# Optimization experiments

Hardware: AMD Instinct MI355X
Metric: run time of the kernel (lower is better)

Reference implementation:

```python
import jax, jax.numpy as jnp
import numpy as np

N = 50000          # nodes
E = 800000         # edges per metapath
P = 4              # metapaths
IN = 256           # in_size
D = 32 * 8         # out_size * layer_num_heads = 256
SEM_H = 128        # SemanticAttention hidden


def setup_inputs() -> dict:
    key = jax.random.key(0)
    ks = jax.random.split(key, 8)
    h = jax.random.normal(ks[0], (N, IN), dtype=jnp.float32)
    src = jax.random.randint(ks[1], (P, E), 0, N, dtype=jnp.int32)
    dst = jax.random.randint(ks[2], (P, E), 0, N, dtype=jnp.int32)
    # per-metapath GraphConv weights (Glorot-ish scale)
    W_gc = jax.random.normal(ks[3], (P, IN, D), dtype=jnp.float32) / np.sqrt(IN)
    b_gc = jnp.zeros((P, D), dtype=jnp.float32)
    # SemanticAttention: Linear(D, SEM_H) -> tanh -> Linear(SEM_H, 1, bias=False)
    W1 = jax.random.normal(ks[4], (D, SEM_H), dtype=jnp.float32) / np.sqrt(D)
    b1 = jnp.zeros((SEM_H,), dtype=jnp.float32)
    w2 = jax.random.normal(ks[5], (SEM_H,), dtype=jnp.float32) / np.sqrt(SEM_H)
    return {"h": h, "src": src, "dst": dst, "W_gc": W_gc, "b_gc": b_gc,
            "W1": W1, "b1": b1, "w2": w2}


def _graph_conv(h, src, dst, W, b):
    # DGL GraphConv with norm='both': D_dst^{-1/2} A D_src^{-1/2} (h W) + b
    ones = jnp.ones((src.shape[0],), dtype=h.dtype)
    deg_out = jnp.clip(jax.ops.segment_sum(ones, src, num_segments=N), 1.0)
    deg_in = jnp.clip(jax.ops.segment_sum(ones, dst, num_segments=N), 1.0)
    x = (h @ W) * jax.lax.rsqrt(deg_out)[:, None]          # [N, D]
    agg = jax.ops.segment_sum(x[src], dst, num_segments=N)  # gather-scatter [N, D]
    return agg * jax.lax.rsqrt(deg_in)[:, None] + b


def reference(h, src, dst, W_gc, b_gc, W1, b1, w2):
    # per-metapath GraphConv (fixed small loop over P metapaths)
    zs = [_graph_conv(h, src[p], dst[p], W_gc[p], b_gc[p]) for p in range(P)]
    z = jnp.stack(zs, axis=1)                               # [N, P, D]
    # SemanticAttention: project -> mean over nodes -> softmax over metapaths
    s = jnp.tanh(z @ W1 + b1) @ w2                          # [N, P]
    beta = jax.nn.softmax(s.mean(axis=0), axis=0)           # [P]
    return jnp.einsum('npd,p->nd', z, beta)                 # [N, D]
```

## Files before the change

kernel.cpp:

```cpp
#include <hip/hip_runtime.h>

#define NN 50000
#define NE 800000
#define NP 4
#define DIN 256
#define DD 256
#define NH 128
#define SA 40
#define NSEG 16
#define SEGE (NE / NSEG)
#define FCH 8192
#define NFC 7
#define SPAD(k) ((k) + ((k) >> 5))

typedef __attribute__((ext_vector_type(8))) short bf16x8;
typedef __attribute__((ext_vector_type(4))) float f32x4;

__device__ __forceinline__ unsigned short f2bf(float f) {
  unsigned u = __float_as_uint(f);
  u += 0x7fff + ((u >> 16) & 1);
  return (unsigned short)(u >> 16);
}
__device__ __forceinline__ float bfl(unsigned u) { return __uint_as_float(u << 16); }
__device__ __forceinline__ float bfh(unsigned u) { return __uint_as_float(u & 0xffff0000u); }


__global__ __launch_bounds__(256) void hist2d_kernel(const int* __restrict__ idx,
                                                     int* __restrict__ cnt) {
  int bx = blockIdx.x;
  int c = bx % NFC, s = bx / NFC;
  int p = blockIdx.y;
  int base = c * FCH, nk = min(FCH, NN - base);
  __shared__ int hs[FCH];
  for (int k = threadIdx.x; k < FCH; k += 256) hs[k] = 0;
  __syncthreads();
  const int4* a4 = (const int4*)(idx + (size_t)p * NE + (size_t)s * SEGE);
  for (int i = threadIdx.x; i < SEGE / 4; i += 256) {
    int4 v = a4[i];
    int k;
    k = v.x - base; if ((unsigned)k < (unsigned)nk) atomicAdd(&hs[k], 1);
    k = v.y - base; if ((unsigned)k < (unsigned)nk) atomicAdd(&hs[k], 1);
    k = v.z - base; if ((unsigned)k < (unsigned)nk) atomicAdd(&hs[k], 1);
    k = v.w - base; if ((unsigned)k < (unsigned)nk) atomicAdd(&hs[k], 1);
  }
  __syncthreads();
  int* out = cnt + (size_t)(p * NSEG + s) * NN + base;
  for (int k = threadIdx.x; k < nk; k += 256) out[k] = hs[k];
}


__global__ __launch_bounds__(1024) void scanA_kernel(
    int* __restrict__ cntD, const int* __restrict__ cntS,
    float* __restrict__ rin, float* __restrict__ rout,
    int* __restrict__ row_ptr, int* __restrict__ chunkdeg) {
  int c = blockIdx.x, p = blockIdx.y;
  int base = c * FCH, nk = min(FCH, NN - base);
  __shared__ int sdeg[FCH + (FCH >> 5)];
  __shared__ int wtot[16], wexc[16];
  int t = threadIdx.x;
  for (int kk = t; kk < FCH; kk += 1024) {
    int run = 0;
    if (kk < nk) {
      size_t o = (size_t)(p * NSEG) * NN + base + kk;
      for (int s = 0; s < NSEG; ++s) {
        size_t oo = o + (size_t)s * NN;
        int v = cntD[oo];
        cntD[oo] = run;
        run += v;
      }
      rin[(size_t)p * NN + base + kk] = rsqrtf((float)max(run, 1));
      int rs = 0;
      for (int s = 0; s < NSEG; ++s) rs += cntS[o + (size_t)s * NN];
      rout[(size_t)p * NN + base + kk] = rsqrtf((float)max(rs, 1));
    }
    sdeg[SPAD(kk)] = run;
  }
  __syncthreads();
  int loc[8];
  int ssum = 0;
#pragma unroll
  for (int j = 0; j < 8; ++j) { loc[j] = ssum; ssum += sdeg[SPAD(t * 8 + j)]; }
  int incl = ssum;
  int lane = t & 63, w = t >> 6;
#pragma unroll
  for (int o = 1; o < 64; o <<= 1) {
    int v = __shfl_up(incl, o);
    if (lane >= o) incl += v;
  }
  if (lane == 63) wtot[w] = incl;
  __syncthreads();
  if (t == 0) {
    int r = 0;
    for (int i = 0; i < 16; ++i) { wexc[i] = r; r += wtot[i]; }
  }
  __syncthreads();
  int tbase = wexc[w] + incl - ssum;
  int* rp = row_ptr + (size_t)p * (NN + 1) + base;
#pragma unroll
  for (int j = 0; j < 8; ++j) {
    int k = t * 8 + j;
    if (k < nk) rp[k] = tbase + loc[j];
  }
  if (t == 1023) chunkdeg[p * NFC + c] = tbase + ssum;
}


__global__ void scanB_kernel(const int* __restrict__ chunkdeg, int* __restrict__ chunk_base,
                             int* __restrict__ row_ptr) {
  int t = threadIdx.x;
  if (t < NP) {
    int run = 0;
    for (int c = 0; c < NFC; ++c) { chunk_base[t * NFC + c] = run; run += chunkdeg[t * NFC + c]; }
    row_ptr[(size_t)t * (NN + 1) + NN] = NE;
  }
}

__global__ __launch_bounds__(1024) void rpfin_kernel(int* __restrict__ row_ptr,
                                                     const int* __restrict__ chunk_base) {
  int k = blockIdx.x * 1024 + threadIdx.x, p = blockIdx.y;
  if (k < NN) row_ptr[(size_t)p * (NN + 1) + k] += chunk_base[p * NFC + (k >> 13)];
}


__global__ __launch_bounds__(256) void scatter_kernel(
    const int* __restrict__ src, const int* __restrict__ dst,
    const int* __restrict__ cntD, const int* __restrict__ row_ptr, int* __restrict__ col) {
  int bx = blockIdx.x;
  int c = bx % NFC, s = bx / NFC;
  int p = blockIdx.y;
  int base = c * FCH, nk = min(FCH, NN - base);
  __shared__ int cur[FCH];
  for (int k = threadIdx.x; k < nk; k += 256)
    cur[k] = row_ptr[(size_t)p * (NN + 1) + base + k] +
             cntD[(size_t)(p * NSEG + s) * NN + base + k];
  __syncthreads();
  const int4* d4 = (const int4*)(dst + (size_t)p * NE + (size_t)s * SEGE);
  const int4* s4 = (const int4*)(src + (size_t)p * NE + (size_t)s * SEGE);
  int* colp = col + (size_t)p * NE;
  for (int i = threadIdx.x; i < SEGE / 4; i += 256) {
    int4 dv = d4[i];
    int4 sv = s4[i];
    int k;
    k = dv.x - base; if ((unsigned)k < (unsigned)nk) colp[atomicAdd(&cur[k], 1)] = sv.x;
    k = dv.y - base; if ((unsigned)k < (unsigned)nk) colp[atomicAdd(&cur[k], 1)] = sv.y;
    k = dv.z - base; if ((unsigned)k < (unsigned)nk) colp[atomicAdd(&cur[k], 1)] = sv.z;
    k = dv.w - base; if ((unsigned)k < (unsigned)nk) colp[atomicAdd(&cur[k], 1)] = sv.w;
  }
}


__global__ void cvt_h_kernel(const float4* __restrict__ h4, ushort4* __restrict__ h2) {
  int i = blockIdx.x * blockDim.x + threadIdx.x;
  if (i >= NN * DIN / 4) return;
  float4 v = h4[i];
  ushort4 o;
  o.x = f2bf(v.x); o.y = f2bf(v.y); o.z = f2bf(v.z); o.w = f2bf(v.w);
  h2[i] = o;
}


__global__ __launch_bounds__(256) void agg_kernel(
    const ushort* __restrict__ h2, const int* __restrict__ col,
    const int* __restrict__ row_ptr, const float* __restrict__ rout,
    const float* __restrict__ rin, ushort* __restrict__ g) {
  int p = blockIdx.y;
  int v = blockIdx.x * 4 + (threadIdx.x >> 6);
  int lane = threadIdx.x & 63;
  const int* colp = col + (size_t)p * NE;
  const float* rop = rout + (size_t)p * NN;
  int beg = row_ptr[p * (NN + 1) + v], end = row_ptr[p * (NN + 1) + v + 1];
  const uint2* hv = (const uint2*)h2;
  float a0 = 0, a1 = 0, a2 = 0, a3 = 0, b0 = 0, b1 = 0, b2 = 0, b3 = 0;
  int j = beg;
  for (; j + 1 < end; j += 2) {
    int s0 = colp[j], s1 = colp[j + 1];
    float r0 = rop[s0], r1 = rop[s1];
    uint2 u0 = hv[(size_t)s0 * 64 + lane];
    uint2 u1 = hv[(size_t)s1 * 64 + lane];
    a0 = fmaf(r0, bfl(u0.x), a0); a1 = fmaf(r0, bfh(u0.x), a1);
    a2 = fmaf(r0, bfl(u0.y), a2); a3 = fmaf(r0, bfh(u0.y), a3);
    b0 = fmaf(r1, bfl(u1.x), b0); b1 = fmaf(r1, bfh(u1.x), b1);
    b2 = fmaf(r1, bfl(u1.y), b2); b3 = fmaf(r1, bfh(u1.y), b3);
  }
  if (j < end) {
    int s0 = colp[j];
    float r0 = rop[s0];
    uint2 u0 = hv[(size_t)s0 * 64 + lane];
    a0 = fmaf(r0, bfl(u0.x), a0); a1 = fmaf(r0, bfh(u0.x), a1);
    a2 = fmaf(r0, bfl(u0.y), a2); a3 = fmaf(r0, bfh(u0.y), a3);
  }
  float ri = rin[(size_t)p * NN + v];
  ushort4 o;
  o.x = f2bf((a0 + b0) * ri); o.y = f2bf((a1 + b1) * ri);
  o.z = f2bf((a2 + b2) * ri); o.w = f2bf((a3 + b3) * ri);
  ((ushort4*)(g + ((size_t)p * NN + v) * DIN))[lane] = o;
}


__global__ void wmul_kernel(const float* __restrict__ Wgc, const float* __restrict__ W1,
                            ushort* __restrict__ Mt) {
  int p = blockIdx.y, k = blockIdx.x, j = threadIdx.x;
  const float* wrow = Wgc + ((size_t)p * DIN + k) * DD;
  float s = 0.f;
  for (int d = 0; d < DD; ++d) s = fmaf(wrow[d], W1[(size_t)d * NH + j], s);
  Mt[((size_t)p * NH + j) * DIN + k] = f2bf(s);
}

__global__ void cvec_kernel(const float* __restrict__ bgc, const float* __restrict__ W1,
                            const float* __restrict__ b1, float* __restrict__ cvec) {
  int p = blockIdx.x, j = threadIdx.x;
  const float* b = bgc + (size_t)p * DD;
  float s = b1[j];
  for (int d = 0; d < DD; ++d) s = fmaf(b[d], W1[(size_t)d * NH + j], s);
  cvec[p * NH + j] = s;
}


__global__ __launch_bounds__(256) void gemm_sem(
    const ushort* __restrict__ g, const ushort* __restrict__ Mt,
    const float* __restrict__ cvec, const float* __restrict__ w2,
    float* __restrict__ ssum) {
  __shared__ ushort As[128 * SA];
  __shared__ ushort Bs[128 * SA];
  __shared__ float wsumf[4];
  const int tid = threadIdx.x;
  const int p = blockIdx.y;
  const int row0 = blockIdx.x * 128;
  const int wave = tid >> 6, lane = tid & 63;
  const int wr = wave >> 1, wc = wave & 1;
  const int srow = tid >> 2, sseg = tid & 3;
  const int fr = lane & 15, fk = (lane >> 4) * 8;
  const ushort* Ag = g + (size_t)p * NN * DIN;
  const ushort* Bg = Mt + (size_t)p * NH * DIN;
  int ar0 = row0 + srow; if (ar0 >= NN) ar0 = NN - 1;
  int ar1 = row0 + srow + 64; if (ar1 >= NN) ar1 = NN - 1;
  f32x4 acc[4][4] = {};
  for (int k2 = 0; k2 < DIN; k2 += 32) {
    uint4 av0 = *(const uint4*)(Ag + (size_t)ar0 * DIN + k2 + sseg * 8);
    uint4 av1 = *(const uint4*)(Ag + (size_t)ar1 * DIN + k2 + sseg * 8);
    uint4 bv0 = *(const uint4*)(Bg + (size_t)srow * DIN + k2 + sseg * 8);
    uint4 bv1 = *(const uint4*)(Bg + (size_t)(srow + 64) * DIN + k2 + sseg * 8);
    __syncthreads();
    *(uint4*)&As[srow * SA + sseg * 8] = av0;
    *(uint4*)&As[(srow + 64) * SA + sseg * 8] = av1;
    *(uint4*)&Bs[srow * SA + sseg * 8] = bv0;
    *(uint4*)&Bs[(srow + 64) * SA + sseg * 8] = bv1;
    __syncthreads();
    bf16x8 af[4], bfv[4];
#pragma unroll
    for (int t = 0; t < 4; ++t) {
      af[t] = *(const bf16x8*)&As[(wr * 64 + t * 16 + fr) * SA + fk];
      bfv[t] = *(const bf16x8*)&Bs[(wc * 64 + t * 16 + fr) * SA + fk];
    }
#pragma unroll
    for (int mt = 0; mt < 4; ++mt)
#pragma unroll
      for (int nt = 0; nt < 4; ++nt)
        acc[mt][nt] = __builtin_amdgcn_mfma_f32_16x16x32_bf16(af[mt], bfv[nt], acc[mt][nt], 0, 0, 0);
  }
  float s = 0.f;
#pragma unroll
  for (int nt = 0; nt < 4; ++nt) {
    int c = wc * 64 + nt * 16 + fr;
    float cc = cvec[p * NH + c];
    float ww = w2[c];
#pragma unroll
    for (int mt = 0; mt < 4; ++mt)
#pragma unroll
      for (int i = 0; i < 4; ++i) {
        int r = row0 + wr * 64 + mt * 16 + (lane >> 4) * 4 + i;
        if (r < NN) {
          float x = acc[mt][nt][i] + cc;
          x = fminf(fmaxf(x, -15.f), 15.f);
          float e = __expf(2.f * x);
          s = fmaf((e - 1.f) / (e + 1.f), ww, s);
        }
      }
  }
#pragma unroll
  for (int o = 32; o > 0; o >>= 1) s += __shfl_down(s, o);
  if (lane == 0) wsumf[wave] = s;
  __syncthreads();
  if (tid == 0) atomicAdd(&ssum[p], wsumf[0] + wsumf[1] + wsumf[2] + wsumf[3]);
}


__global__ void beta_kernel(const float* __restrict__ ssum, const float* __restrict__ bgc,
                            float* __restrict__ beta, float* __restrict__ bout) {
  __shared__ float sb[NP];
  if (threadIdx.x == 0) {
    float m[NP];
    float mx = -1e30f;
    for (int p = 0; p < NP; ++p) {
      m[p] = ssum[p] / (float)NN;
      mx = fmaxf(mx, m[p]);
    }
    float tot = 0.f;
    for (int p = 0; p < NP; ++p) { m[p] = expf(m[p] - mx); tot += m[p]; }
    for (int p = 0; p < NP; ++p) { sb[p] = m[p] / tot; beta[p] = sb[p]; }
  }
  __syncthreads();
  int d = threadIdx.x;
  float s = 0.f;
  for (int p = 0; p < NP; ++p) s = fmaf(sb[p], bgc[p * DD + d], s);
  bout[d] = s;
}

__global__ void scaleWt_kernel(const float* __restrict__ Wgc, const float* __restrict__ beta,
                               ushort* __restrict__ Wt) {
  int i = blockIdx.x * blockDim.x + threadIdx.x;
  if (i >= DD * NP * DIN) return;
  int n = i >> 10;
  int pk = i & 1023;
  int p = pk >> 8, k = pk & 255;
  Wt[i] = f2bf(beta[p] * Wgc[((size_t)p * DIN + k) * DD + n]);
}


__global__ __launch_bounds__(256) void gemm_main(
    const ushort* __restrict__ g, const ushort* __restrict__ Wt,
    const float* __restrict__ bout, float* __restrict__ out) {
  __shared__ ushort As[128 * SA];
  __shared__ ushort Bs[128 * SA];
  const int tid = threadIdx.x;
  const int row0 = blockIdx.x * 128;
  const int col0 = blockIdx.y * 128;
  const int wave = tid >> 6, lane = tid & 63;
  const int wr = wave >> 1, wc = wave & 1;
  const int srow = tid >> 2, sseg = tid & 3;
  const int fr = lane & 15, fk = (lane >> 4) * 8;
  int ar0 = row0 + srow; if (ar0 >= NN) ar0 = NN - 1;
  int ar1 = row0 + srow + 64; if (ar1 >= NN) ar1 = NN - 1;
  f32x4 acc[4][4] = {};
  for (int p = 0; p < NP; ++p) {
    const ushort* Ag = g + (size_t)p * NN * DIN;
    for (int k2 = 0; k2 < DIN; k2 += 32) {
      uint4 av0 = *(const uint4*)(Ag + (size_t)ar0 * DIN + k2 + sseg * 8);
      uint4 av1 = *(const uint4*)(Ag + (size_t)ar1 * DIN + k2 + sseg * 8);
      uint4 bv0 = *(const uint4*)(Wt + (size_t)(col0 + srow) * (NP * DIN) + p * DIN + k2 + sseg * 8);
      uint4 bv1 = *(const uint4*)(Wt + (size_t)(col0 + srow + 64) * (NP * DIN) + p * DIN + k2 + sseg * 8);
      __syncthreads();
      *(uint4*)&As[srow * SA + sseg * 8] = av0;
      *(uint4*)&As[(srow + 64) * SA + sseg * 8] = av1;
      *(uint4*)&Bs[srow * SA + sseg * 8] = bv0;
      *(uint4*)&Bs[(srow + 64) * SA + sseg * 8] = bv1;
      __syncthreads();
      bf16x8 af[4], bfv[4];
#pragma unroll
      for (int t = 0; t < 4; ++t) {
        af[t] = *(const bf16x8*)&As[(wr * 64 + t * 16 + fr) * SA + fk];
        bfv[t] = *(const bf16x8*)&Bs[(wc * 64 + t * 16 + fr) * SA + fk];
      }
#pragma unroll
      for (int mt = 0; mt < 4; ++mt)
#pragma unroll
        for (int nt = 0; nt < 4; ++nt)
          acc[mt][nt] = __builtin_amdgcn_mfma_f32_16x16x32_bf16(af[mt], bfv[nt], acc[mt][nt], 0, 0, 0);
    }
  }
#pragma unroll
  for (int nt = 0; nt < 4; ++nt) {
    int c = col0 + wc * 64 + nt * 16 + fr;
    float bb = bout[c];
#pragma unroll
    for (int mt = 0; mt < 4; ++mt)
#pragma unroll
      for (int i = 0; i < 4; ++i) {
        int r = row0 + wr * 64 + mt * 16 + (lane >> 4) * 4 + i;
        if (r < NN) out[(size_t)r * DD + c] = acc[mt][nt][i] + bb;
      }
  }
}


extern "C" void kernel_launch(void* const* d_in, const int* in_sizes, int n_in,
                              void* d_out, int out_size, void* d_ws, size_t ws_size,
                              hipStream_t stream) {
  const float* h = (const float*)d_in[0];
  const int* src = (const int*)d_in[1];
  const int* dst = (const int*)d_in[2];
  const float* Wgc = (const float*)d_in[3];
  const float* bgc = (const float*)d_in[4];
  const float* W1 = (const float*)d_in[5];
  const float* b1 = (const float*)d_in[6];
  const float* w2 = (const float*)d_in[7];
  float* out = (float*)d_out;

  char* base = (char*)d_ws;
  size_t off = 0;
  auto alloc = [&](size_t bytes) -> char* {
    char* ptr = base + off;
    off = (off + bytes + 255) & ~(size_t)255;
    return ptr;
  };
  int* cntD = (int*)alloc((size_t)NP * NSEG * NN * sizeof(int));
  int* cntS = (int*)alloc((size_t)NP * NSEG * NN * sizeof(int));
  float* rin = (float*)alloc((size_t)NP * NN * sizeof(float));
  float* rout = (float*)alloc((size_t)NP * NN * sizeof(float));
  int* row_ptr = (int*)alloc((size_t)NP * (NN + 1) * sizeof(int));
  int* chunkdeg = (int*)alloc((size_t)NP * NFC * sizeof(int));
  int* chunk_base = (int*)alloc((size_t)NP * NFC * sizeof(int));
  ushort* h2 = (ushort*)alloc((size_t)NN * DIN * sizeof(ushort));
  ushort* g = (ushort*)alloc((size_t)NP * NN * DIN * sizeof(ushort));
  ushort* Mt = (ushort*)alloc((size_t)NP * NH * DIN * sizeof(ushort));
  ushort* Wt = (ushort*)alloc((size_t)DD * NP * DIN * sizeof(ushort));
  float* cvec = (float*)alloc((size_t)NP * NH * sizeof(float));
  float* ssum = (float*)alloc(NP * sizeof(float));
  float* beta = (float*)alloc(NP * sizeof(float));
  float* bout = (float*)alloc(DD * sizeof(float));
  int* colbuf = (int*)cntS;
  if (off > ws_size) return;

  hipMemsetAsync(ssum, 0, NP * sizeof(float), stream);

  hist2d_kernel<<<dim3(NFC * NSEG, NP), 256, 0, stream>>>(dst, cntD);
  hist2d_kernel<<<dim3(NFC * NSEG, NP), 256, 0, stream>>>(src, cntS);
  scanA_kernel<<<dim3(NFC, NP), 1024, 0, stream>>>(cntD, cntS, rin, rout, row_ptr, chunkdeg);
  scanB_kernel<<<1, 64, 0, stream>>>(chunkdeg, chunk_base, row_ptr);
  rpfin_kernel<<<dim3((NN + 1023) / 1024, NP), 1024, 0, stream>>>(row_ptr, chunk_base);
  cvt_h_kernel<<<(NN * DIN / 4 + 255) / 256, 256, 0, stream>>>((const float4*)h, (ushort4*)h2);
  scatter_kernel<<<dim3(NFC * NSEG, NP), 256, 0, stream>>>(src, dst, cntD, row_ptr, colbuf);
  agg_kernel<<<dim3(NN / 4, NP), 256, 0, stream>>>(h2, colbuf, row_ptr, rout, rin, g);
  wmul_kernel<<<dim3(DIN, NP), NH, 0, stream>>>(Wgc, W1, Mt);
  cvec_kernel<<<NP, NH, 0, stream>>>(bgc, W1, b1, cvec);
  gemm_sem<<<dim3((NN + 127) / 128, NP), 256, 0, stream>>>(g, Mt, cvec, w2, ssum);
  beta_kernel<<<1, 256, 0, stream>>>(ssum, bgc, beta, bout);
  scaleWt_kernel<<<(DD * NP * DIN + 255) / 256, 256, 0, stream>>>(Wgc, beta, Wt);
  gemm_main<<<dim3((NN + 127) / 128, 2), 256, 0, stream>>>(g, Wt, bout, out);
}
```

Before: 656.6 us.

## Use global-atomic CSR build, batched-index gather with packed FMA, reorder GEMM grid

Replaces the segmented shared-memory histogram and scatter, which scan all edges seven times per chunk, with single-pass global-atomic degree counting and a global-atomic scatter into a separate column buffer. The aggregation kernel now stages up to 64 neighbor indices and weights per wave in shared memory, issues 8 gathers at once, and accumulates with packed v_pk_fma_f32. The main GEMM grid is transposed so the two column tiles of a row block run next to each other and can share A in L2. The cost is global atomic contention and a nondeterministic edge order within each CSR row, plus two extra memsets.

```diff
diff --git a/kernel.cpp b/kernel.cpp
--- a/kernel.cpp
+++ b/kernel.cpp
@@ -7,50 +7,51 @@
 #define DD 256
 #define NH 128
 #define SA 40
-#define NSEG 16
-#define SEGE (NE / NSEG)
 #define FCH 8192
 #define NFC 7
 #define SPAD(k) ((k) + ((k) >> 5))
 
 typedef __attribute__((ext_vector_type(8))) short bf16x8;
 typedef __attribute__((ext_vector_type(4))) float f32x4;
+typedef __attribute__((ext_vector_type(2))) float f32x2;
 
 __device__ __forceinline__ unsigned short f2bf(float f) {
   unsigned u = __float_as_uint(f);
   u += 0x7fff + ((u >> 16) & 1);
   return (unsigned short)(u >> 16);
 }
-__device__ __forceinline__ float bfl(unsigned u) { return __uint_as_float(u << 16); }
-__device__ __forceinline__ float bfh(unsigned u) { return __uint_as_float(u & 0xffff0000u); }
-
-
-__global__ __launch_bounds__(256) void hist2d_kernel(const int* __restrict__ idx,
-                                                     int* __restrict__ cnt) {
-  int bx = blockIdx.x;
-  int c = bx % NFC, s = bx / NFC;
-  int p = blockIdx.y;
-  int base = c * FCH, nk = min(FCH, NN - base);
-  __shared__ int hs[FCH];
-  for (int k = threadIdx.x; k < FCH; k += 256) hs[k] = 0;
-  __syncthreads();
-  const int4* a4 = (const int4*)(idx + (size_t)p * NE + (size_t)s * SEGE);
-  for (int i = threadIdx.x; i < SEGE / 4; i += 256) {
-    int4 v = a4[i];
-    int k;
-    k = v.x - base; if ((unsigned)k < (unsigned)nk) atomicAdd(&hs[k], 1);
-    k = v.y - base; if ((unsigned)k < (unsigned)nk) atomicAdd(&hs[k], 1);
-    k = v.z - base; if ((unsigned)k < (unsigned)nk) atomicAdd(&hs[k], 1);
-    k = v.w - base; if ((unsigned)k < (unsigned)nk) atomicAdd(&hs[k], 1);
-  }
-  __syncthreads();
-  int* out = cnt + (size_t)(p * NSEG + s) * NN + base;
-  for (int k = threadIdx.x; k < nk; k += 256) out[k] = hs[k];
+
+__device__ __forceinline__ f32x2 unpk(unsigned u) {
+  f32x2 f;
+  f.x = __uint_as_float(u << 16);
+  f.y = __uint_as_float(u & 0xffff0000u);
+  return f;
+}
+__device__ __forceinline__ void pkfma(f32x2& acc, f32x2 m, f32x2 v) {
+  asm("v_pk_fma_f32 %0, %1, %2, %0" : "+v"(acc) : "v"(m), "v"(v));
+}
+
+
+__global__ __launch_bounds__(256) void deg_kernel(const int* __restrict__ src,
+                                                  const int* __restrict__ dst,
+                                                  int* __restrict__ degS,
+                                                  int* __restrict__ degD) {
+  int i = blockIdx.x * 256 + threadIdx.x;
+  if (i >= NP * NE / 4) return;
+  int p = i / (NE / 4);
+  int4 dv = ((const int4*)dst)[i];
+  int4 sv = ((const int4*)src)[i];
+  int* dd = degD + (size_t)p * NN;
+  int* so = degS + (size_t)p * NN;
+  atomicAdd(&dd[dv.x], 1); atomicAdd(&dd[dv.y], 1);
+  atomicAdd(&dd[dv.z], 1); atomicAdd(&dd[dv.w], 1);
+  atomicAdd(&so[sv.x], 1); atomicAdd(&so[sv.y], 1);
+  atomicAdd(&so[sv.z], 1); atomicAdd(&so[sv.w], 1);
 }
 
 
 __global__ __launch_bounds__(1024) void scanA_kernel(
-    int* __restrict__ cntD, const int* __restrict__ cntS,
+    const int* __restrict__ degD, const int* __restrict__ degS,
     float* __restrict__ rin, float* __restrict__ rout,
     int* __restrict__ row_ptr, int* __restrict__ chunkdeg) {
   int c = blockIdx.x, p = blockIdx.y;
@@ -59,21 +60,15 @@
   __shared__ int wtot[16], wexc[16];
   int t = threadIdx.x;
   for (int kk = t; kk < FCH; kk += 1024) {
-    int run = 0;
+    int dI = 0;
     if (kk < nk) {
-      size_t o = (size_t)(p * NSEG) * NN + base + kk;
-      for (int s = 0; s < NSEG; ++s) {
-        size_t oo = o + (size_t)s * NN;
-        int v = cntD[oo];
-        cntD[oo] = run;
-        run += v;
-      }
-      rin[(size_t)p * NN + base + kk] = rsqrtf((float)max(run, 1));
-      int rs = 0;
-      for (int s = 0; s < NSEG; ++s) rs += cntS[o + (size_t)s * NN];
-      rout[(size_t)p * NN + base + kk] = rsqrtf((float)max(rs, 1));
+      size_t o = (size_t)p * NN + base + kk;
+      dI = degD[o];
+      int dO = degS[o];
+      rin[o] = rsqrtf((float)max(dI, 1));
+      rout[o] = rsqrtf((float)max(dO, 1));
     }
-    sdeg[SPAD(kk)] = run;
+    sdeg[SPAD(kk)] = dI;
   }
   __syncthreads();
   int loc[8];
@@ -116,36 +111,31 @@
 }
 
 __global__ __launch_bounds__(1024) void rpfin_kernel(int* __restrict__ row_ptr,
-                                                     const int* __restrict__ chunk_base) {
+                                                     const int* __restrict__ chunk_base,
+                                                     int* __restrict__ cur) {
   int k = blockIdx.x * 1024 + threadIdx.x, p = blockIdx.y;
-  if (k < NN) row_ptr[(size_t)p * (NN + 1) + k] += chunk_base[p * NFC + (k >> 13)];
-}
-
-
-__global__ __launch_bounds__(256) void scatter_kernel(
+  if (k < NN) {
+    int v = row_ptr[(size_t)p * (NN + 1) + k] + chunk_base[p * NFC + (k >> 13)];
+    row_ptr[(size_t)p * (NN + 1) + k] = v;
+    cur[(size_t)p * NN + k] = v;
+  }
+}
+
+
+__global__ __launch_bounds__(256) void scatter2_kernel(
     const int* __restrict__ src, const int* __restrict__ dst,
-    const int* __restrict__ cntD, const int* __restrict__ row_ptr, int* __restrict__ col) {
-  int bx = blockIdx.x;
-  int c = bx % NFC, s = bx / NFC;
-  int p = blockIdx.y;
-  int base = c * FCH, nk = min(FCH, NN - base);
-  __shared__ int cur[FCH];
-  for (int k = threadIdx.x; k < nk; k += 256)
-    cur[k] = row_ptr[(size_t)p * (NN + 1) + base + k] +
-             cntD[(size_t)(p * NSEG + s) * NN + base + k];
-  __syncthreads();
-  const int4* d4 = (const int4*)(dst + (size_t)p * NE + (size_t)s * SEGE);
-  const int4* s4 = (const int4*)(src + (size_t)p * NE + (size_t)s * SEGE);
+    int* __restrict__ cur, int* __restrict__ col) {
+  int i = blockIdx.x * 256 + threadIdx.x;
+  if (i >= NP * NE / 4) return;
+  int p = i / (NE / 4);
+  int4 dv = ((const int4*)dst)[i];
+  int4 sv = ((const int4*)src)[i];
+  int* curp = cur + (size_t)p * NN;
   int* colp = col + (size_t)p * NE;
-  for (int i = threadIdx.x; i < SEGE / 4; i += 256) {
-    int4 dv = d4[i];
-    int4 sv = s4[i];
-    int k;
-    k = dv.x - base; if ((unsigned)k < (unsigned)nk) colp[atomicAdd(&cur[k], 1)] = sv.x;
-    k = dv.y - base; if ((unsigned)k < (unsigned)nk) colp[atomicAdd(&cur[k], 1)] = sv.y;
-    k = dv.z - base; if ((unsigned)k < (unsigned)nk) colp[atomicAdd(&cur[k], 1)] = sv.z;
-    k = dv.w - base; if ((unsigned)k < (unsigned)nk) colp[atomicAdd(&cur[k], 1)] = sv.w;
-  }
+  colp[atomicAdd(&curp[dv.x], 1)] = sv.x;
+  colp[atomicAdd(&curp[dv.y], 1)] = sv.y;
+  colp[atomicAdd(&curp[dv.z], 1)] = sv.z;
+  colp[atomicAdd(&curp[dv.w], 1)] = sv.w;
 }
 
 
@@ -163,36 +153,53 @@
     const ushort* __restrict__ h2, const int* __restrict__ col,
     const int* __restrict__ row_ptr, const float* __restrict__ rout,
     const float* __restrict__ rin, ushort* __restrict__ g) {
+  __shared__ int2 sW[4][64];
   int p = blockIdx.y;
   int v = blockIdx.x * 4 + (threadIdx.x >> 6);
   int lane = threadIdx.x & 63;
+  int wv = threadIdx.x >> 6;
   const int* colp = col + (size_t)p * NE;
   const float* rop = rout + (size_t)p * NN;
   int beg = row_ptr[p * (NN + 1) + v], end = row_ptr[p * (NN + 1) + v + 1];
-  const uint2* hv = (const uint2*)h2;
-  float a0 = 0, a1 = 0, a2 = 0, a3 = 0, b0 = 0, b1 = 0, b2 = 0, b3 = 0;
-  int j = beg;
-  for (; j + 1 < end; j += 2) {
-    int s0 = colp[j], s1 = colp[j + 1];
-    float r0 = rop[s0], r1 = rop[s1];
-    uint2 u0 = hv[(size_t)s0 * 64 + lane];
-    uint2 u1 = hv[(size_t)s1 * 64 + lane];
-    a0 = fmaf(r0, bfl(u0.x), a0); a1 = fmaf(r0, bfh(u0.x), a1);
-    a2 = fmaf(r0, bfl(u0.y), a2); a3 = fmaf(r0, bfh(u0.y), a3);
-    b0 = fmaf(r1, bfl(u1.x), b0); b1 = fmaf(r1, bfh(u1.x), b1);
-    b2 = fmaf(r1, bfl(u1.y), b2); b3 = fmaf(r1, bfh(u1.y), b3);
-  }
-  if (j < end) {
-    int s0 = colp[j];
-    float r0 = rop[s0];
-    uint2 u0 = hv[(size_t)s0 * 64 + lane];
-    a0 = fmaf(r0, bfl(u0.x), a0); a1 = fmaf(r0, bfh(u0.x), a1);
-    a2 = fmaf(r0, bfl(u0.y), a2); a3 = fmaf(r0, bfh(u0.y), a3);
+  const char* hb = (const char*)h2 + (size_t)lane * 8;
+  f32x2 accA0 = {0.f, 0.f}, accA1 = {0.f, 0.f};
+  f32x2 accB0 = {0.f, 0.f}, accB1 = {0.f, 0.f};
+  for (int j0 = beg; j0 < end; j0 += 64) {
+    int nw = end - j0;
+    if (nw > 64) nw = 64;
+    int cv = 0;
+    float rv = 0.f;
+    if (lane < nw) { cv = colp[j0 + lane]; rv = rop[cv]; }
+    sW[wv][lane] = make_int2(cv, __float_as_int(rv));
+    int nwb = (nw + 7) & ~7;
+    for (int t = 0; t < nwb; t += 8) {
+      int2 w[8];
+#pragma unroll
+      for (int q = 0; q < 8; ++q) w[q] = sW[wv][t + q];
+      uint2 u[8];
+#pragma unroll
+      for (int q = 0; q < 8; ++q)
+        u[q] = *(const uint2*)(hb + ((size_t)(unsigned)w[q].x << 9));
+#pragma unroll
+      for (int q = 0; q < 8; ++q) {
+        float r = __int_as_float(w[q].y);
+        f32x2 rr = {r, r};
+        if (q & 1) {
+          pkfma(accB0, rr, unpk(u[q].x));
+          pkfma(accB1, rr, unpk(u[q].y));
+        } else {
+          pkfma(accA0, rr, unpk(u[q].x));
+          pkfma(accA1, rr, unpk(u[q].y));
+        }
+      }
+    }
   }
   float ri = rin[(size_t)p * NN + v];
+  f32x2 s0 = accA0 + accB0;
+  f32x2 s1 = accA1 + accB1;
   ushort4 o;
-  o.x = f2bf((a0 + b0) * ri); o.y = f2bf((a1 + b1) * ri);
-  o.z = f2bf((a2 + b2) * ri); o.w = f2bf((a3 + b3) * ri);
+  o.x = f2bf(s0.x * ri); o.y = f2bf(s0.y * ri);
+  o.z = f2bf(s1.x * ri); o.w = f2bf(s1.y * ri);
   ((ushort4*)(g + ((size_t)p * NN + v) * DIN))[lane] = o;
 }
 
@@ -323,8 +330,8 @@
   __shared__ ushort As[128 * SA];
   __shared__ ushort Bs[128 * SA];
   const int tid = threadIdx.x;
-  const int row0 = blockIdx.x * 128;
-  const int col0 = blockIdx.y * 128;
+  const int row0 = blockIdx.y * 128;
+  const int col0 = blockIdx.x * 128;
   const int wave = tid >> 6, lane = tid & 63;
   const int wr = wave >> 1, wc = wave & 1;
   const int srow = tid >> 2, sseg = tid & 3;
@@ -393,13 +400,15 @@
     off = (off + bytes + 255) & ~(size_t)255;
     return ptr;
   };
-  int* cntD = (int*)alloc((size_t)NP * NSEG * NN * sizeof(int));
-  int* cntS = (int*)alloc((size_t)NP * NSEG * NN * sizeof(int));
+  int* degD = (int*)alloc((size_t)NP * NN * sizeof(int));
+  int* degS = (int*)alloc((size_t)NP * NN * sizeof(int));
   float* rin = (float*)alloc((size_t)NP * NN * sizeof(float));
   float* rout = (float*)alloc((size_t)NP * NN * sizeof(float));
   int* row_ptr = (int*)alloc((size_t)NP * (NN + 1) * sizeof(int));
+  int* cur = (int*)alloc((size_t)NP * NN * sizeof(int));
   int* chunkdeg = (int*)alloc((size_t)NP * NFC * sizeof(int));
   int* chunk_base = (int*)alloc((size_t)NP * NFC * sizeof(int));
+  int* colbuf = (int*)alloc((size_t)NP * NE * sizeof(int));
   ushort* h2 = (ushort*)alloc((size_t)NN * DIN * sizeof(ushort));
   ushort* g = (ushort*)alloc((size_t)NP * NN * DIN * sizeof(ushort));
   ushort* Mt = (ushort*)alloc((size_t)NP * NH * DIN * sizeof(ushort));
@@ -408,23 +417,23 @@
   float* ssum = (float*)alloc(NP * sizeof(float));
   float* beta = (float*)alloc(NP * sizeof(float));
   float* bout = (float*)alloc(DD * sizeof(float));
-  int* colbuf = (int*)cntS;
   if (off > ws_size) return;
 
+  hipMemsetAsync(degD, 0, (size_t)NP * NN * sizeof(int), stream);
+  hipMemsetAsync(degS, 0, (size_t)NP * NN * sizeof(int), stream);
   hipMemsetAsync(ssum, 0, NP * sizeof(float), stream);
 
-  hist2d_kernel<<<dim3(NFC * NSEG, NP), 256, 0, stream>>>(dst, cntD);
-  hist2d_kernel<<<dim3(NFC * NSEG, NP), 256, 0, stream>>>(src, cntS);
-  scanA_kernel<<<dim3(NFC, NP), 1024, 0, stream>>>(cntD, cntS, rin, rout, row_ptr, chunkdeg);
+  deg_kernel<<<(NP * NE / 4 + 255) / 256, 256, 0, stream>>>(src, dst, degS, degD);
+  scanA_kernel<<<dim3(NFC, NP), 1024, 0, stream>>>(degD, degS, rin, rout, row_ptr, chunkdeg);
   scanB_kernel<<<1, 64, 0, stream>>>(chunkdeg, chunk_base, row_ptr);
-  rpfin_kernel<<<dim3((NN + 1023) / 1024, NP), 1024, 0, stream>>>(row_ptr, chunk_base);
+  rpfin_kernel<<<dim3((NN + 1023) / 1024, NP), 1024, 0, stream>>>(row_ptr, chunk_base, cur);
   cvt_h_kernel<<<(NN * DIN / 4 + 255) / 256, 256, 0, stream>>>((const float4*)h, (ushort4*)h2);
-  scatter_kernel<<<dim3(NFC * NSEG, NP), 256, 0, stream>>>(src, dst, cntD, row_ptr, colbuf);
+  scatter2_kernel<<<(NP * NE / 4 + 255) / 256, 256, 0, stream>>>(src, dst, cur, colbuf);
   agg_kernel<<<dim3(NN / 4, NP), 256, 0, stream>>>(h2, colbuf, row_ptr, rout, rin, g);
   wmul_kernel<<<dim3(DIN, NP), NH, 0, stream>>>(Wgc, W1, Mt);
   cvec_kernel<<<NP, NH, 0, stream>>>(bgc, W1, b1, cvec);
   gemm_sem<<<dim3((NN + 127) / 128, NP), 256, 0, stream>>>(g, Mt, cvec, w2, ssum);
   beta_kernel<<<1, 256, 0, stream>>>(ssum, bgc, beta, bout);
   scaleWt_kernel<<<(DD * NP * DIN + 255) / 256, 256, 0, stream>>>(Wgc, beta, Wt);
-  gemm_main<<<dim3((NN + 127) / 128, 2), 256, 0, stream>>>(g, Wt, bout, out);
-}
+  gemm_main<<<dim3(2, (NN + 127) / 128), 256, 0, stream>>>(g, Wt, bout, out);
+}
```

After: 975.7 us. +48.6%, slower.

## Batch neighbor indices via LDS in aggregation, widen histogram chunks, reorder gemm grid

Applied to the files above, without the earlier changes.

The aggregation kernel now loads up to 64 neighbor indices and their out-degree scales per wave cooperatively, stages them in shared memory, and issues 8 independent row gathers at a time using packed FMA. This is meant to expose more memory-level parallelism than the serial 2-way unrolled loop. The histogram and scatter kernels use 16K-node chunks instead of 8K, which halves the number of full passes over the edge arrays at the cost of larger LDS use and lower occupancy. The gemm_main grid is transposed so the two column blocks for the same row tile run next to each other, which should improve reuse of the A tile in L2.

```diff
diff --git a/kernel.cpp b/kernel.cpp
--- a/kernel.cpp
+++ b/kernel.cpp
@@ -9,30 +9,41 @@
 #define SA 40
 #define NSEG 16
 #define SEGE (NE / NSEG)
-#define FCH 8192
-#define NFC 7
+#define HCH 16384
+#define NHC 4
+#define SCH 8192
+#define NSC 7
 #define SPAD(k) ((k) + ((k) >> 5))
 
 typedef __attribute__((ext_vector_type(8))) short bf16x8;
 typedef __attribute__((ext_vector_type(4))) float f32x4;
+typedef __attribute__((ext_vector_type(2))) float f32x2;
 
 __device__ __forceinline__ unsigned short f2bf(float f) {
   unsigned u = __float_as_uint(f);
   u += 0x7fff + ((u >> 16) & 1);
   return (unsigned short)(u >> 16);
 }
-__device__ __forceinline__ float bfl(unsigned u) { return __uint_as_float(u << 16); }
-__device__ __forceinline__ float bfh(unsigned u) { return __uint_as_float(u & 0xffff0000u); }
+
+__device__ __forceinline__ f32x2 unpk(unsigned u) {
+  f32x2 f;
+  f.x = __uint_as_float(u << 16);
+  f.y = __uint_as_float(u & 0xffff0000u);
+  return f;
+}
+__device__ __forceinline__ void pkfma(f32x2& acc, f32x2 m, f32x2 v) {
+  asm("v_pk_fma_f32 %0, %1, %2, %0" : "+v"(acc) : "v"(m), "v"(v));
+}
 
 
 __global__ __launch_bounds__(256) void hist2d_kernel(const int* __restrict__ idx,
                                                      int* __restrict__ cnt) {
   int bx = blockIdx.x;
-  int c = bx % NFC, s = bx / NFC;
+  int c = bx % NHC, s = bx / NHC;
   int p = blockIdx.y;
-  int base = c * FCH, nk = min(FCH, NN - base);
-  __shared__ int hs[FCH];
-  for (int k = threadIdx.x; k < FCH; k += 256) hs[k] = 0;
+  int base = c * HCH, nk = min(HCH, NN - base);
+  __shared__ int hs[HCH];
+  for (int k = threadIdx.x; k < HCH; k += 256) hs[k] = 0;
   __syncthreads();
   const int4* a4 = (const int4*)(idx + (size_t)p * NE + (size_t)s * SEGE);
   for (int i = threadIdx.x; i < SEGE / 4; i += 256) {
@@ -54,11 +65,11 @@
     float* __restrict__ rin, float* __restrict__ rout,
     int* __restrict__ row_ptr, int* __restrict__ chunkdeg) {
   int c = blockIdx.x, p = blockIdx.y;
-  int base = c * FCH, nk = min(FCH, NN - base);
-  __shared__ int sdeg[FCH + (FCH >> 5)];
+  int base = c * SCH, nk = min(SCH, NN - base);
+  __shared__ int sdeg[SCH + (SCH >> 5)];
   __shared__ int wtot[16], wexc[16];
   int t = threadIdx.x;
-  for (int kk = t; kk < FCH; kk += 1024) {
+  for (int kk = t; kk < SCH; kk += 1024) {
     int run = 0;
     if (kk < nk) {
       size_t o = (size_t)(p * NSEG) * NN + base + kk;
@@ -101,7 +112,7 @@
     int k = t * 8 + j;
     if (k < nk) rp[k] = tbase + loc[j];
   }
-  if (t == 1023) chunkdeg[p * NFC + c] = tbase + ssum;
+  if (t == 1023) chunkdeg[p * NSC + c] = tbase + ssum;
 }
 
 
@@ -110,7 +121,7 @@
   int t = threadIdx.x;
   if (t < NP) {
     int run = 0;
-    for (int c = 0; c < NFC; ++c) { chunk_base[t * NFC + c] = run; run += chunkdeg[t * NFC + c]; }
+    for (int c = 0; c < NSC; ++c) { chunk_base[t * NSC + c] = run; run += chunkdeg[t * NSC + c]; }
     row_ptr[(size_t)t * (NN + 1) + NN] = NE;
   }
 }
@@ -118,7 +129,7 @@
 __global__ __launch_bounds__(1024) void rpfin_kernel(int* __restrict__ row_ptr,
                                                      const int* __restrict__ chunk_base) {
   int k = blockIdx.x * 1024 + threadIdx.x, p = blockIdx.y;
-  if (k < NN) row_ptr[(size_t)p * (NN + 1) + k] += chunk_base[p * NFC + (k >> 13)];
+  if (k < NN) row_ptr[(size_t)p * (NN + 1) + k] += chunk_base[p * NSC + (k >> 13)];
 }
 
 
@@ -126,10 +137,10 @@
     const int* __restrict__ src, const int* __restrict__ dst,
     const int* __restrict__ cntD, const int* __restrict__ row_ptr, int* __restrict__ col) {
   int bx = blockIdx.x;
-  int c = bx % NFC, s = bx / NFC;
+  int c = bx % NHC, s = bx / NHC;
   int p = blockIdx.y;
-  int base = c * FCH, nk = min(FCH, NN - base);
-  __shared__ int cur[FCH];
+  int base = c * HCH, nk = min(HCH, NN - base);
+  __shared__ int cur[HCH];
   for (int k = threadIdx.x; k < nk; k += 256)
     cur[k] = row_ptr[(size_t)p * (NN + 1) + base + k] +
              cntD[(size_t)(p * NSEG + s) * NN + base + k];
@@ -163,36 +174,53 @@
     const ushort* __restrict__ h2, const int* __restrict__ col,
     const int* __restrict__ row_ptr, const float* __restrict__ rout,
     const float* __restrict__ rin, ushort* __restrict__ g) {
+  __shared__ int2 sW[4][64];
   int p = blockIdx.y;
   int v = blockIdx.x * 4 + (threadIdx.x >> 6);
   int lane = threadIdx.x & 63;
+  int wv = threadIdx.x >> 6;
   const int* colp = col + (size_t)p * NE;
   const float* rop = rout + (size_t)p * NN;
   int beg = row_ptr[p * (NN + 1) + v], end = row_ptr[p * (NN + 1) + v + 1];
-  const uint2* hv = (const uint2*)h2;
-  float a0 = 0, a1 = 0, a2 = 0, a3 = 0, b0 = 0, b1 = 0, b2 = 0, b3 = 0;
-  int j = beg;
-  for (; j + 1 < end; j += 2) {
-    int s0 = colp[j], s1 = colp[j + 1];
-    float r0 = rop[s0], r1 = rop[s1];
-    uint2 u0 = hv[(size_t)s0 * 64 + lane];
-    uint2 u1 = hv[(size_t)s1 * 64 + lane];
-    a0 = fmaf(r0, bfl(u0.x), a0); a1 = fmaf(r0, bfh(u0.x), a1);
-    a2 = fmaf(r0, bfl(u0.y), a2); a3 = fmaf(r0, bfh(u0.y), a3);
-    b0 = fmaf(r1, bfl(u1.x), b0); b1 = fmaf(r1, bfh(u1.x), b1);
-    b2 = fmaf(r1, bfl(u1.y), b2); b3 = fmaf(r1, bfh(u1.y), b3);
-  }
-  if (j < end) {
-    int s0 = colp[j];
-    float r0 = rop[s0];
-    uint2 u0 = hv[(size_t)s0 * 64 + lane];
-    a0 = fmaf(r0, bfl(u0.x), a0); a1 = fmaf(r0, bfh(u0.x), a1);
-    a2 = fmaf(r0, bfl(u0.y), a2); a3 = fmaf(r0, bfh(u0.y), a3);
+  const char* hb = (const char*)h2 + (size_t)lane * 8;
+  f32x2 accA0 = {0.f, 0.f}, accA1 = {0.f, 0.f};
+  f32x2 accB0 = {0.f, 0.f}, accB1 = {0.f, 0.f};
+  for (int j0 = beg; j0 < end; j0 += 64) {
+    int nw = end - j0;
+    if (nw > 64) nw = 64;
+    int cv = 0;
+    float rv = 0.f;
+    if (lane < nw) { cv = colp[j0 + lane]; rv = rop[cv]; }
+    sW[wv][lane] = make_int2(cv, __float_as_int(rv));
+    int nwb = (nw + 7) & ~7;
+    for (int t = 0; t < nwb; t += 8) {
+      int2 w[8];
+#pragma unroll
+      for (int q = 0; q < 8; ++q) w[q] = sW[wv][t + q];
+      uint2 u[8];
+#pragma unroll
+      for (int q = 0; q < 8; ++q)
+        u[q] = *(const uint2*)(hb + ((size_t)(unsigned)w[q].x << 9));
+#pragma unroll
+      for (int q = 0; q < 8; ++q) {
+        float r = __int_as_float(w[q].y);
+        f32x2 rr = {r, r};
+        if (q & 1) {
+          pkfma(accB0, rr, unpk(u[q].x));
+          pkfma(accB1, rr, unpk(u[q].y));
+        } else {
+          pkfma(accA0, rr, unpk(u[q].x));
+          pkfma(accA1, rr, unpk(u[q].y));
+        }
+      }
+    }
   }
   float ri = rin[(size_t)p * NN + v];
+  f32x2 s0 = accA0 + accB0;
+  f32x2 s1 = accA1 + accB1;
   ushort4 o;
-  o.x = f2bf((a0 + b0) * ri); o.y = f2bf((a1 + b1) * ri);
-  o.z = f2bf((a2 + b2) * ri); o.w = f2bf((a3 + b3) * ri);
+  o.x = f2bf(s0.x * ri); o.y = f2bf(s0.y * ri);
+  o.z = f2bf(s1.x * ri); o.w = f2bf(s1.y * ri);
   ((ushort4*)(g + ((size_t)p * NN + v) * DIN))[lane] = o;
 }
 
@@ -323,8 +351,8 @@
   __shared__ ushort As[128 * SA];
   __shared__ ushort Bs[128 * SA];
   const int tid = threadIdx.x;
-  const int row0 = blockIdx.x * 128;
-  const int col0 = blockIdx.y * 128;
+  const int row0 = blockIdx.y * 128;
+  const int col0 = blockIdx.x * 128;
   const int wave = tid >> 6, lane = tid & 63;
   const int wr = wave >> 1, wc = wave & 1;
   const int srow = tid >> 2, sseg = tid & 3;
@@ -398,8 +426,8 @@
   float* rin = (float*)alloc((size_t)NP * NN * sizeof(float));
   float* rout = (float*)alloc((size_t)NP * NN * sizeof(float));
   int* row_ptr = (int*)alloc((size_t)NP * (NN + 1) * sizeof(int));
-  int* chunkdeg = (int*)alloc((size_t)NP * NFC * sizeof(int));
-  int* chunk_base = (int*)alloc((size_t)NP * NFC * sizeof(int));
+  int* chunkdeg = (int*)alloc((size_t)NP * NSC * sizeof(int));
+  int* chunk_base = (int*)alloc((size_t)NP * NSC * sizeof(int));
   ushort* h2 = (ushort*)alloc((size_t)NN * DIN * sizeof(ushort));
   ushort* g = (ushort*)alloc((size_t)NP * NN * DIN * sizeof(ushort));
   ushort* Mt = (ushort*)alloc((size_t)NP * NH * DIN * sizeof(ushort));
@@ -413,18 +441,18 @@
 
   hipMemsetAsync(ssum, 0, NP * sizeof(float), stream);
 
-  hist2d_kernel<<<dim3(NFC * NSEG, NP), 256, 0, stream>>>(dst, cntD);
-  hist2d_kernel<<<dim3(NFC * NSEG, NP), 256, 0, stream>>>(src, cntS);
-  scanA_kernel<<<dim3(NFC, NP), 1024, 0, stream>>>(cntD, cntS, rin, rout, row_ptr, chunkdeg);
+  hist2d_kernel<<<dim3(NHC * NSEG, NP), 256, 0, stream>>>(dst, cntD);
+  hist2d_kernel<<<dim3(NHC * NSEG, NP), 256, 0, stream>>>(src, cntS);
+  scanA_kernel<<<dim3(NSC, NP), 1024, 0, stream>>>(cntD, cntS, rin, rout, row_ptr, chunkdeg);
   scanB_kernel<<<1, 64, 0, stream>>>(chunkdeg, chunk_base, row_ptr);
   rpfin_kernel<<<dim3((NN + 1023) / 1024, NP), 1024, 0, stream>>>(row_ptr, chunk_base);
   cvt_h_kernel<<<(NN * DIN / 4 + 255) / 256, 256, 0, stream>>>((const float4*)h, (ushort4*)h2);
-  scatter_kernel<<<dim3(NFC * NSEG, NP), 256, 0, stream>>>(src, dst, cntD, row_ptr, colbuf);
+  scatter_kernel<<<dim3(NHC * NSEG, NP), 256, 0, stream>>>(src, dst, cntD, row_ptr, colbuf);
   agg_kernel<<<dim3(NN / 4, NP), 256, 0, stream>>>(h2, colbuf, row_ptr, rout, rin, g);
   wmul_kernel<<<dim3(DIN, NP), NH, 0, stream>>>(Wgc, W1, Mt);
   cvec_kernel<<<NP, NH, 0, stream>>>(bgc, W1, b1, cvec);
   gemm_sem<<<dim3((NN + 127) / 128, NP), 256, 0, stream>>>(g, Mt, cvec, w2, ssum);
   beta_kernel<<<1, 256, 0, stream>>>(ssum, bgc, beta, bout);
   scaleWt_kernel<<<(DD * NP * DIN + 255) / 256, 256, 0, stream>>>(Wgc, beta, Wt);
-  gemm_main<<<dim3((NN + 127) / 128, 2), 256, 0, stream>>>(g, Wt, bout, out);
-}
+  gemm_main<<<dim3(2, (NN + 127) / 128), 256, 0, stream>>>(g, Wt, bout, out);
+}
```

Measured after the change: 631.0 us. 3.9% less time.
